# Performance work log

Measured on AMD Instinct MI355X. Metric: run time of the kernel, lower is better.

The kernel has to match this reference:

```python
import jax, jax.numpy as jnp
import numpy as np

VOCAB = 50257
EMB = 512


def setup_inputs() -> dict:
    key = jax.random.key(0)
    k1, k2, k3 = jax.random.split(key, 3)
    input_token_ids = jax.random.randint(k1, (8, 4096), 0, VOCAB, dtype=jnp.int64 if jax.config.jax_enable_x64 else jnp.int32)
    W = jax.random.normal(k2, (EMB, VOCAB), dtype=jnp.float32)  # nn.Linear(vocab, emb).weight
    b = jax.random.normal(k3, (EMB,), dtype=jnp.float32)        # nn.Linear bias
    return {"input_token_ids": input_token_ids, "W": W, "b": b}


def reference(input_token_ids, W, b):
    # one_hot(ids, V) @ W.T + b  ==  W.T[ids] + b   (exact same math, gather form)
    scale = jnp.asarray(EMB, W.dtype) ** 0.5
    emb = jnp.take(W.T, input_token_ids, axis=0)  # [B, S, EMB]
    return (emb + b) * scale
```

## Files before the change

### kernel.cpp

```cpp
#include <hip/hip_runtime.h>
#include <hip/hip_bf16.h>


constexpr int VOCAB = 50257;
constexpr int EMB   = 512;
constexpr int NTOK  = 8 * 4096;
constexpr float SCALE = 22.62741699796952f;

constexpr int VB  = 32;
constexpr int NB  = (VOCAB + VB - 1) / VB;
constexpr int CAP = 128;
constexpr int ECH = 256;


__global__ __launch_bounds__(256) void init_counts(int* __restrict__ counts) {
    int i = blockIdx.x * 256 + threadIdx.x;
    if (i < NB + 1) counts[i] = 0;
}

__global__ __launch_bounds__(256) void build_buckets(
    const int* __restrict__ ids,
    int* __restrict__ counts,
    int* __restrict__ olist,
    int* __restrict__ buckets)
{
    int t = blockIdx.x * 256 + threadIdx.x;
    int id = ids[t];
    int bkt = id >> 5;
    int slot = atomicAdd(&counts[bkt], 1);
    if (slot < CAP) {
        buckets[bkt * CAP + slot] = (t << 5) | (id & 31);
    } else {
        int o = atomicAdd(&counts[NB], 1);
        olist[o] = t;
    }
}

__global__ __launch_bounds__(256) void scatter_main(
    const float* __restrict__ W,
    const float* __restrict__ bias,
    const float* __restrict__ bias_scaled,
    const int*   __restrict__ counts,
    const int*   __restrict__ buckets,
    float*       __restrict__ out)
{
    __shared__ float tile[(ECH / 2) * 65];
    __shared__ int   toks[CAP];
    __shared__ int   s_cnt;

    int b   = blockIdx.x;
    int v0  = b * VB;
    int tid = threadIdx.x;

    if (tid == 0) s_cnt = counts[b];
    if (tid < CAP) toks[tid] = buckets[b * CAP + tid];
    __syncthreads();
    int cnt = min(s_cnt, CAP);
    if (cnt == 0) return;

    int lane = tid & 63;
    int w    = tid >> 6;
    int tx   = tid & 31;

    int v = v0 + tx;
    bool vok = v < VOCAB;

    for (int chunk = 0; chunk < EMB / ECH; ++chunk) {
        int e0 = chunk * ECH;

        #pragma unroll
        for (int p = 0; p < ECH / 8; ++p) {
            int el = p * 8 + 2 * w + (lane >> 5);
            size_t gidx = (size_t)(e0 + el) * VOCAB + v;
            if (!vok) gidx = 0;
            const float* gp = W + gidx;
            float* lp = &tile[(p * 4 + w) * 65];
            __builtin_amdgcn_global_load_lds(
                (const __attribute__((address_space(1))) void*)gp,
                (__attribute__((address_space(3))) void*)lp, 4, 0, 0);
        }
        __syncthreads();

        for (int i = w; i < cnt; i += 4) {
            int pk = toks[i];
            int t  = pk >> 5;
            int vl = pk & 31;
            int g0 = 2 * lane;
            float4 o;
            o.x = tile[g0 * 65 + vl];
            o.y = tile[g0 * 65 + 32 + vl];
            o.z = tile[(g0 + 1) * 65 + vl];
            o.w = tile[(g0 + 1) * 65 + 32 + vl];
            int e = e0 + 4 * lane;
            o.x = (o.x + bias[e + 0]) * SCALE;
            o.y = (o.y + bias[e + 1]) * SCALE;
            o.z = (o.z + bias[e + 2]) * SCALE;
            o.w = (o.w + bias[e + 3]) * SCALE;
            *reinterpret_cast<float4*>(out + (size_t)t * EMB + e) = o;
        }
        __syncthreads();
    }
}

__global__ __launch_bounds__(256) void overflow_fix(
    const int*   __restrict__ counts,
    const int*   __restrict__ olist,
    const int*   __restrict__ ids,
    const float* __restrict__ W,
    const float* __restrict__ bias,
    float*       __restrict__ out)
{
    int n    = counts[NB];
    int wid  = (blockIdx.x * 256 + threadIdx.x) >> 6;
    int lane = threadIdx.x & 63;
    int nw   = (gridDim.x * 256) >> 6;
    for (int ww = wid; ww < n; ww += nw) {
        int t  = olist[ww];
        int id = ids[t];
        #pragma unroll
        for (int m = 0; m < 8; ++m) {
            int e = lane + m * 64;
            out[(size_t)t * EMB + e] = (W[(size_t)e * VOCAB + id] + bias[e]) * SCALE;
        }
    }
}

__global__ __launch_bounds__(256) void embed_gather(
    const int*   __restrict__ ids,
    const float* __restrict__ W,
    const float* __restrict__ b,
    float*       __restrict__ out)
{
    int idx4 = blockIdx.x * blockDim.x + threadIdx.x;
    int t    = idx4 >> 7;
    int e    = (idx4 & 127) << 2;
    int id = ids[t];
    float4 bb = *reinterpret_cast<const float4*>(b + e);
    const float* wcol = W + (size_t)id;
    float4 o;
    o.x = (wcol[(size_t)(e + 0) * VOCAB] + bb.x) * SCALE;
    o.y = (wcol[(size_t)(e + 1) * VOCAB] + bb.y) * SCALE;
    o.z = (wcol[(size_t)(e + 2) * VOCAB] + bb.z) * SCALE;
    o.w = (wcol[(size_t)(e + 3) * VOCAB] + bb.w) * SCALE;
    *reinterpret_cast<float4*>(out + (size_t)idx4 * 4) = o;
}

extern "C" void kernel_launch(void* const* d_in, const int* in_sizes, int n_in,
                              void* d_out, int out_size, void* d_ws, size_t ws_size,
                              hipStream_t stream)
{
    const int*   ids  = (const int*)  d_in[0];
    const float* W    = (const float*)d_in[1];
    const float* bias = (const float*)d_in[2];
    float*       out  = (float*)d_out;

    const size_t ws_ints_needed = (size_t)NB + 1 + NTOK + (size_t)NB * CAP;

    if (ws_size >= ws_ints_needed * sizeof(int)) {
        int* counts  = (int*)d_ws;
        int* olist   = counts + NB + 1;
        int* buckets = olist + NTOK;

        init_counts<<<(NB + 1 + 255) / 256, 256, 0, stream>>>(counts);
        build_buckets<<<NTOK / 256, 256, 0, stream>>>(ids, counts, olist, buckets);
        scatter_main<<<NB, 256, 0, stream>>>(W, bias, nullptr, counts, buckets, out);
        overflow_fix<<<32, 256, 0, stream>>>(counts, olist, ids, W, bias, out);
    } else {
        constexpr int total4 = NTOK * EMB / 4;
        embed_gather<<<total4 / 256, 256, 0, stream>>>(ids, W, bias, out);
    }
}
```

Before: 189.8 us.

## Widen vocab buckets and double-buffer W chunks with async LDS loads

Buckets now cover 64 vocab columns and the embedding dimension is staged in eight 64-row chunks, double-buffered in shared memory. The next chunk's global_load_lds is issued before the current one is consumed, using explicit vmcnt waits and raw barriers. Each lane writes one scalar per token with nontemporal stores, bias is preloaded into registers, and the counts init kernel is replaced by hipMemsetAsync. The goal is to overlap W streaming with output writes and halve the block count. The cost is scalar instead of float4 stores and a smaller bucket capacity that sends more tokens to the overflow path.

```diff
diff --git a/kernel.cpp b/kernel.cpp
--- a/kernel.cpp
+++ b/kernel.cpp
@@ -1,5 +1,4 @@
 #include <hip/hip_runtime.h>
-#include <hip/hip_bf16.h>
 
 
 constexpr int VOCAB = 50257;
@@ -7,16 +6,13 @@
 constexpr int NTOK  = 8 * 4096;
 constexpr float SCALE = 22.62741699796952f;
 
-constexpr int VB  = 32;
+constexpr int VB  = 64;
 constexpr int NB  = (VOCAB + VB - 1) / VB;
-constexpr int CAP = 128;
-constexpr int ECH = 256;
+constexpr int CAP = 96;
+constexpr int ECH = 64;
+constexpr int NCH = EMB / ECH;
+constexpr int RS  = VB + 1;
 
-
-__global__ __launch_bounds__(256) void init_counts(int* __restrict__ counts) {
-    int i = blockIdx.x * 256 + threadIdx.x;
-    if (i < NB + 1) counts[i] = 0;
-}
 
 __global__ __launch_bounds__(256) void build_buckets(
     const int* __restrict__ ids,
@@ -26,79 +22,82 @@
 {
     int t = blockIdx.x * 256 + threadIdx.x;
     int id = ids[t];
-    int bkt = id >> 5;
+    int bkt = id >> 6;
     int slot = atomicAdd(&counts[bkt], 1);
     if (slot < CAP) {
-        buckets[bkt * CAP + slot] = (t << 5) | (id & 31);
+        buckets[bkt * CAP + slot] = (t << 6) | (id & 63);
     } else {
         int o = atomicAdd(&counts[NB], 1);
         olist[o] = t;
     }
 }
 
-__global__ __launch_bounds__(256) void scatter_main(
+__global__ __launch_bounds__(256, 4) void scatter_main(
     const float* __restrict__ W,
     const float* __restrict__ bias,
-    const float* __restrict__ bias_scaled,
     const int*   __restrict__ counts,
     const int*   __restrict__ buckets,
     float*       __restrict__ out)
 {
-    __shared__ float tile[(ECH / 2) * 65];
+    __shared__ float buf[2][ECH * RS];
     __shared__ int   toks[CAP];
     __shared__ int   s_cnt;
 
-    int b   = blockIdx.x;
-    int v0  = b * VB;
-    int tid = threadIdx.x;
+    const int b    = blockIdx.x;
+    const int tid  = threadIdx.x;
+    const int lane = tid & 63;
+    const int w    = tid >> 6;
 
     if (tid == 0) s_cnt = counts[b];
     if (tid < CAP) toks[tid] = buckets[b * CAP + tid];
+
+    float bb[NCH];
+    #pragma unroll
+    for (int c = 0; c < NCH; ++c) bb[c] = bias[c * ECH + lane];
+
+    int v = b * VB + lane;
+    const float* wsrc = W + (v < VOCAB ? v : VOCAB - 1);
+
     __syncthreads();
-    int cnt = min(s_cnt, CAP);
+    const int cnt = min(s_cnt, CAP);
     if (cnt == 0) return;
 
-    int lane = tid & 63;
-    int w    = tid >> 6;
-    int tx   = tid & 31;
-
-    int v = v0 + tx;
-    bool vok = v < VOCAB;
-
-    for (int chunk = 0; chunk < EMB / ECH; ++chunk) {
-        int e0 = chunk * ECH;
-
+    auto stage = [&](int c, int sel) {
         #pragma unroll
-        for (int p = 0; p < ECH / 8; ++p) {
-            int el = p * 8 + 2 * w + (lane >> 5);
-            size_t gidx = (size_t)(e0 + el) * VOCAB + v;
-            if (!vok) gidx = 0;
-            const float* gp = W + gidx;
-            float* lp = &tile[(p * 4 + w) * 65];
+        for (int p = 0; p < 16; ++p) {
+            const int rr = w * 16 + p;
+            const float* gp = wsrc + (size_t)(c * ECH + rr) * VOCAB;
+            float* lp = &buf[sel][rr * RS];
             __builtin_amdgcn_global_load_lds(
                 (const __attribute__((address_space(1))) void*)gp,
                 (__attribute__((address_space(3))) void*)lp, 4, 0, 0);
         }
-        __syncthreads();
+    };
 
+    stage(0, 0);
+
+    #pragma unroll
+    for (int c = 0; c < NCH; ++c) {
+        const int sel = c & 1;
+        if (c + 1 < NCH) {
+            stage(c + 1, sel ^ 1);
+            asm volatile("s_waitcnt vmcnt(16)" ::: "memory");
+        } else {
+            asm volatile("s_waitcnt vmcnt(0)" ::: "memory");
+        }
+        __builtin_amdgcn_s_barrier();
+
+        const float  bc    = bb[c];
+        const float* tilec = &buf[sel][lane * RS];
+        float*       orow  = out + c * ECH + lane;
         for (int i = w; i < cnt; i += 4) {
-            int pk = toks[i];
-            int t  = pk >> 5;
-            int vl = pk & 31;
-            int g0 = 2 * lane;
-            float4 o;
-            o.x = tile[g0 * 65 + vl];
-            o.y = tile[g0 * 65 + 32 + vl];
-            o.z = tile[(g0 + 1) * 65 + vl];
-            o.w = tile[(g0 + 1) * 65 + 32 + vl];
-            int e = e0 + 4 * lane;
-            o.x = (o.x + bias[e + 0]) * SCALE;
-            o.y = (o.y + bias[e + 1]) * SCALE;
-            o.z = (o.z + bias[e + 2]) * SCALE;
-            o.w = (o.w + bias[e + 3]) * SCALE;
-            *reinterpret_cast<float4*>(out + (size_t)t * EMB + e) = o;
+            const int pk = toks[i];
+            const int t  = pk >> 6;
+            const int vl = pk & 63;
+            __builtin_nontemporal_store((tilec[vl] + bc) * SCALE,
+                                        orow + (size_t)t * EMB);
         }
-        __syncthreads();
+        if (c + 1 < NCH) __builtin_amdgcn_s_barrier();
     }
 }
 
@@ -161,9 +160,9 @@
         int* olist   = counts + NB + 1;
         int* buckets = olist + NTOK;
 
-        init_counts<<<(NB + 1 + 255) / 256, 256, 0, stream>>>(counts);
+        hipMemsetAsync(counts, 0, (NB + 1) * sizeof(int), stream);
         build_buckets<<<NTOK / 256, 256, 0, stream>>>(ids, counts, olist, buckets);
-        scatter_main<<<NB, 256, 0, stream>>>(W, bias, nullptr, counts, buckets, out);
+        scatter_main<<<NB, 256, 0, stream>>>(W, bias, counts, buckets, out);
         overflow_fix<<<32, 256, 0, stream>>>(counts, olist, ids, W, bias, out);
     } else {
         constexpr int total4 = NTOK * EMB / 4;
```

New measurement: 199.9 us. +5.4%, slower.
